# Performance work log

Hardware: AMD Instinct MI355X
Metric: run time of the kernel (lower is better)

The kernel has to match this reference:

```python
import jax, jax.numpy as jnp
import numpy as np

B = 4096
FEAT = 512
EMB = 64
HID = 1024
NUM_CLASSES = 64   # == option_num == noise_lib_Y.shape[0]
LIB_X = 256
LIB_Y = 256
OUT_J = 256


def setup_inputs() -> dict:
    key = jax.random.key(0)
    ks = jax.random.split(key, 16)
    s = lambda k, shape, fan: jax.random.normal(k, shape, jnp.float32) / np.sqrt(fan)
    d_in = FEAT + EMB
    return {
        "state": jax.random.normal(ks[0], (B, FEAT), jnp.float32),
        "option": jax.random.randint(ks[1], (B,), 0, NUM_CLASSES, jnp.int64),
        "embed_table": s(ks[2], (NUM_CLASSES, EMB), EMB),
        "Wx1": s(ks[3], (d_in, HID), d_in), "bx1": jnp.zeros((HID,), jnp.float32),
        "Wx2": s(ks[4], (HID, LIB_X), HID), "bx2": jnp.zeros((LIB_X,), jnp.float32),
        "Wy1": s(ks[5], (d_in, HID), d_in), "by1": jnp.zeros((HID,), jnp.float32),
        "Wy2": s(ks[6], (HID, LIB_Y), HID), "by2": jnp.zeros((LIB_Y,), jnp.float32),
        "noise_lib_X": s(ks[7], (LIB_X, OUT_J), LIB_X),
        "noise_lib_Y": s(ks[8], (NUM_CLASSES, LIB_Y, OUT_J), LIB_Y),
    }


def _mlp(x, W1, b1, W2, b2):
    # MLP_RELU, layer_num=2: Linear -> ReLU -> Linear
    h = jax.nn.relu(x @ W1 + b1)
    return h @ W2 + b2


def reference(state, option, embed_table, Wx1, bx1, Wx2, bx2,
              Wy1, by1, Wy2, by2, noise_lib_X, noise_lib_Y):
    option_embed = embed_table[option]                      # [B, EMB]
    all_state = jnp.concatenate([state, option_embed], axis=-1)
    cls_X = _mlp(all_state, Wx1, bx1, Wx2, bx2)             # [B, LIB_X]
    cls_Y = _mlp(all_state, Wy1, by1, Wy2, by2)             # [B, LIB_Y]
    # Original: einsum('bi,mij->bmj') then mask with one_hot(option).
    # Mathematically identical gather-then-matmul (honors the routing sparsity):
    noise_Y_sel = noise_lib_Y[option]                       # [B, LIB_Y, OUT_J]
    generate_noise_Y = jnp.einsum('bi,bij->bj', cls_Y, noise_Y_sel)
    generate_noise_X = cls_X @ noise_lib_X                  # [B, OUT_J]
    return (generate_noise_X, generate_noise_Y)
```

## Files before the change

kernel.cpp:

```cpp
#include <hip/hip_runtime.h>

typedef unsigned short u16;
typedef unsigned int u32;

using f32x4  = __attribute__((ext_vector_type(4))) float;
using bf16x8 = __attribute__((ext_vector_type(8))) __bf16;

#define DEV __device__ __forceinline__

DEV u16 f2bf(float f) {
  union { float f; u32 u; } x; x.f = f;
  return (u16)((x.u + 0x7fffu + ((x.u >> 16) & 1u)) >> 16);
}
DEV float bf2f(u16 h) {
  union { u32 u; float f; } x; x.u = ((u32)h) << 16;
  return x.f;
}

DEV void async_cp16(const u16* g, u16* l) {
  __builtin_amdgcn_global_load_lds((const __attribute__((address_space(1))) void*)g,
                                   (__attribute__((address_space(3))) void*)l,
                                   16, 0, 0);
}

static constexpr int BATCH = 4096;
static constexpr int FEAT  = 512;
static constexpr int EMB   = 64;
static constexpr int HID   = 1024;
static constexpr int NC    = 64;
static constexpr int DIN   = 576;
static constexpr int LIB   = 256;

DEV void detect_lite(const u32* __restrict__ sraw, const u32* __restrict__ oraw,
                     int* isf32, int* ostr) {
  __shared__ int cib, conz;
  const int t = threadIdx.x;
  if (t == 0) { cib = 0; conz = 0; }
  u32 w = sraw[t];
  u32 e = (w >> 7) & 0xFFu;
  unsigned long long m1 = __ballot(e >= 100 && e <= 142);
  unsigned long long m2 = __ballot((t & 1) && oraw[t] != 0);
  __syncthreads();
  if ((t & 63) == 0) {
    atomicAdd(&cib, __popcll(m1));
    atomicAdd(&conz, __popcll(m2));
  }
  __syncthreads();
  *isf32 = (cib < 128) ? 1 : 0;
  *ostr  = (conz == 0) ? 2 : 1;
}

DEV void load16_bf(u16* v, const void* __restrict__ in, size_t off, int isf32) {
  if (isf32) {
    const float4* s = (const float4*)((const float*)in + off);
    float4 a0 = s[0], a1 = s[1], a2 = s[2], a3 = s[3];
    v[0] = f2bf(a0.x); v[1] = f2bf(a0.y); v[2]  = f2bf(a0.z); v[3]  = f2bf(a0.w);
    v[4] = f2bf(a1.x); v[5] = f2bf(a1.y); v[6]  = f2bf(a1.z); v[7]  = f2bf(a1.w);
    v[8] = f2bf(a2.x); v[9] = f2bf(a2.y); v[10] = f2bf(a2.z); v[11] = f2bf(a2.w);
    v[12] = f2bf(a3.x); v[13] = f2bf(a3.y); v[14] = f2bf(a3.z); v[15] = f2bf(a3.w);
  } else {
    const uint4* s = (const uint4*)((const u16*)in + off);
    *(uint4*)&v[0] = s[0];
    *(uint4*)&v[8] = s[1];
  }
}

DEV void do_transpose64(u16* lds, const void* __restrict__ in,
                        u16* __restrict__ out, int R, int C,
                        int by, int bx, int isf32) {
  u16* tile = lds;
  const int t = threadIdx.x;
  {
    const int r = t >> 2, c0 = (t & 3) * 16;
    u16 v[16];
    load16_bf(v, in, (size_t)(by * 64 + r) * C + (bx * 64 + c0), isf32);
    *(uint4*)&tile[r * 72 + c0]     = *(uint4*)&v[0];
    *(uint4*)&tile[r * 72 + c0 + 8] = *(uint4*)&v[8];
  }
  __syncthreads();
  {
    const int c = t & 63, rs = (t >> 6) * 16;
    u16 w[16];
#pragma unroll
    for (int i = 0; i < 16; ++i) w[i] = tile[(rs + i) * 72 + c];
    size_t oo = (size_t)(bx * 64 + c) * R + (by * 64 + rs);
    *(uint4*)&out[oo]     = *(uint4*)&w[0];
    *(uint4*)&out[oo + 8] = *(uint4*)&w[8];
  }
}

DEV void tgemm_task(u16* lds, const void* __restrict__ nX,
                    const void* __restrict__ Wx2, u16* __restrict__ T,
                    int mt, int nt, int isf32) {
  u16* Als = lds;
  u16* Bls = lds + 64 * 72;
  const int t = threadIdx.x;
  const int m0 = mt * 64, q0 = nt * 64;
  const int lane = t & 63, wid = t >> 6;
  const int wm = wid >> 1, wn = wid & 1;
  const int lr = lane & 15, lq = lane >> 4;
  f32x4 acc[2][2] = {};
  for (int k0 = 0; k0 < LIB; k0 += 64) {
    __syncthreads();
    {
      const int r = t >> 2, c0 = (t & 3) * 16;
      u16 v[16];
      load16_bf(v, nX, (size_t)(k0 + r) * LIB + m0 + c0, isf32);
#pragma unroll
      for (int j = 0; j < 16; ++j) Als[(c0 + j) * 72 + r] = v[j];
      const int q = t >> 2, ic = (t & 3) * 16;
      u16 w16[16];
      load16_bf(w16, Wx2, (size_t)(q0 + q) * LIB + k0 + ic, isf32);
      u16* dst = &Bls[((ic >> 5) * 64 + q) * 32 + (ic & 31)];
      *(uint4*)dst       = *(uint4*)&w16[0];
      *(uint4*)(dst + 8) = *(uint4*)&w16[8];
    }
    __syncthreads();
#pragma unroll
    for (int sl = 0; sl < 2; ++sl) {
      bf16x8 av[2], bv[2];
#pragma unroll
      for (int i2 = 0; i2 < 2; ++i2)
        av[i2] = *(const bf16x8*)&Als[(wm * 32 + i2 * 16 + lr) * 72 + sl * 32 + lq * 8];
#pragma unroll
      for (int j2 = 0; j2 < 2; ++j2)
        bv[j2] = *(const bf16x8*)&Bls[(sl * 64 + wn * 32 + j2 * 16 + lr) * 32 + lq * 8];
#pragma unroll
      for (int i2 = 0; i2 < 2; ++i2)
#pragma unroll
        for (int j2 = 0; j2 < 2; ++j2)
          acc[i2][j2] = __builtin_amdgcn_mfma_f32_16x16x32_bf16(av[i2], bv[j2], acc[i2][j2], 0, 0, 0);
    }
  }
#pragma unroll
  for (int j2 = 0; j2 < 2; ++j2) {
    const int gc = q0 + wn * 32 + j2 * 16 + lr;
#pragma unroll
    for (int i2 = 0; i2 < 2; ++i2) {
      const int gr = m0 + wm * 32 + i2 * 16 + lq * 4;
#pragma unroll
      for (int r = 0; r < 4; ++r)
        T[(size_t)(gr + r) * HID + gc] = f2bf(acc[i2][j2][r]);
    }
  }
}

struct PrepArgs {
  const void *state, *emb, *Wx1, *Wy1, *Wy2, *Wx2, *nX, *bx2;
  const int* opt;
  u16 *all_state, *WT1x, *WT1y, *WT2y, *T;
  float* b2x;
};
static constexpr int PB_CONCAT = BATCH * 36 / 256;
static constexpr int PB_WT1 = (DIN / 64) * (HID / 64);
static constexpr int PB_WT2 = (HID / 64) * (LIB / 64);
static constexpr int PB_TG  = (LIB / 64) * (HID / 64);
static constexpr int PB_BIAS = 4;
static constexpr int PREP_BLOCKS = PB_CONCAT + 2 * PB_WT1 + PB_WT2 + PB_TG
                                 + PB_BIAS;

__global__ __launch_bounds__(256) void prep_k(PrepArgs a) {
  __shared__ __align__(16) u16 plds[64 * 72 + 128 * 32];
  __shared__ float red[4][64];
  int isf32, os;
  detect_lite((const u32*)a.state, (const u32*)a.opt, &isf32, &os);
  int bid = blockIdx.x;
  const int t = threadIdx.x;
  if (bid < PB_CONCAT) {
    int idx = bid * 256 + t;
    int b = idx / 36, ch = idx % 36;
    const void* base;
    size_t srcoff;
    if (ch < 32) { base = a.state; srcoff = (size_t)b * FEAT + ch * 16; }
    else {
      base = a.emb;
      srcoff = (size_t)a.opt[(size_t)b * os] * EMB + (ch - 32) * 16;
    }
    u16 o[16];
    load16_bf(o, base, srcoff, isf32);
    u16* dst = a.all_state + (size_t)b * DIN + ch * 16;
    *(uint4*)dst       = *(const uint4*)&o[0];
    *(uint4*)(dst + 8) = *(const uint4*)&o[8];
    return;
  }
  bid -= PB_CONCAT;
  if (bid < PB_WT1) { do_transpose64(plds, a.Wx1, a.WT1x, DIN, HID, bid >> 4, bid & 15, isf32); return; }
  bid -= PB_WT1;
  if (bid < PB_WT1) { do_transpose64(plds, a.Wy1, a.WT1y, DIN, HID, bid >> 4, bid & 15, isf32); return; }
  bid -= PB_WT1;
  if (bid < PB_WT2) { do_transpose64(plds, a.Wy2, a.WT2y, HID, LIB, bid >> 2, bid & 3, isf32); return; }
  bid -= PB_WT2;
  if (bid < PB_TG) { tgemm_task(plds, a.nX, a.Wx2, a.T, bid & 3, bid >> 2, isf32); return; }
  bid -= PB_TG;
  {
    const int j = bid * 64 + (t & 63), g = t >> 6;
    float acc = 0.f;
    for (int ii = 0; ii < 64; ++ii) {
      const int i = g * 64 + ii;
      float s = isf32 ? ((const float*)a.bx2)[i] : bf2f(((const u16*)a.bx2)[i]);
      float v = isf32 ? ((const float*)a.nX)[(size_t)i * LIB + j]
                      : bf2f(((const u16*)a.nX)[(size_t)i * LIB + j]);
      acc += s * v;
    }
    red[g][t & 63] = acc;
    __syncthreads();
    if (g == 0)
      a.b2x[j] = red[0][t & 63] + red[1][t & 63] + red[2][t & 63] + red[3][t & 63];
  }
}

template <int BM, int BN, bool RELU>
DEV void gemm_tile(u16* lds, const u16* __restrict__ A, const u16* __restrict__ Bt,
                   const void* bias, void* C, int N, int K, int m0, int n0,
                   int isf32, bool cf32, bool bf32) {
  constexpr int WM = BM / 2, WN = BN / 2, TM = WM / 16, TN = WN / 16;
  u16* As = lds;
  u16* Bs = lds + BM * 64;
  const int t = threadIdx.x;
  const int lane = t & 63, wid = t >> 6;
  const int wm = wid >> 1, wn = wid & 1;
  const int lr = lane & 15, lq = lane >> 4;
  f32x4 acc[TM][TN] = {};
  for (int k0 = 0; k0 < K; k0 += 64) {
    __syncthreads();
#pragma unroll
    for (int sl = 0; sl < 2; ++sl) {
#pragma unroll
      for (int u = 0; u < BM / 64; ++u) {
        int unit = u * 256 + t;
        int r = unit >> 2, c8 = (unit & 3) * 8;
        async_cp16(A + (size_t)(m0 + r) * K + (k0 + sl * 32 + c8),
                   &As[(sl * BM + r) * 32 + c8]);
      }
#pragma unroll
      for (int u = 0; u < BN / 64; ++u) {
        int unit = u * 256 + t;
        int r = unit >> 2, c8 = (unit & 3) * 8;
        async_cp16(Bt + (size_t)(n0 + r) * K + (k0 + sl * 32 + c8),
                   &Bs[(sl * BN + r) * 32 + c8]);
      }
    }
    __syncthreads();
#pragma unroll
    for (int sl = 0; sl < 2; ++sl) {
      bf16x8 av[TM], bv[TN];
#pragma unroll
      for (int i = 0; i < TM; ++i)
        av[i] = *(const bf16x8*)&As[(sl * BM + wm * WM + i * 16 + lr) * 32 + lq * 8];
#pragma unroll
      for (int j = 0; j < TN; ++j)
        bv[j] = *(const bf16x8*)&Bs[(sl * BN + wn * WN + j * 16 + lr) * 32 + lq * 8];
#pragma unroll
      for (int i = 0; i < TM; ++i)
#pragma unroll
        for (int j = 0; j < TN; ++j)
          acc[i][j] = __builtin_amdgcn_mfma_f32_16x16x32_bf16(av[i], bv[j], acc[i][j], 0, 0, 0);
    }
  }
#pragma unroll
  for (int j = 0; j < TN; ++j) {
    const int gc = n0 + wn * WN + j * 16 + lr;
    const float bval = bias
        ? (bf32 ? ((const float*)bias)[gc] : bf2f(((const u16*)bias)[gc]))
        : 0.f;
#pragma unroll
    for (int i = 0; i < TM; ++i) {
      const int gr = m0 + wm * WM + i * 16 + lq * 4;
#pragma unroll
      for (int r = 0; r < 4; ++r) {
        float v = acc[i][j][r] + bval;
        if (RELU) v = fmaxf(v, 0.f);
        const size_t idx = (size_t)(gr + r) * N + gc;
        if (cf32) ((float*)C)[idx] = v;
        else      ((u16*)C)[idx] = f2bf(v);
      }
    }
  }
}

struct GArg { const u16* A; const u16* Bt; const void* bias; void* C; int cflag; int bflag; };

template <int BM, int BN, bool RELU>
__global__ __launch_bounds__(256) void gemm_bt(GArg g0, GArg g1, int N, int K,
                                               const void* state, const void* opt) {
  __shared__ __align__(16) u16 lds[(BM + BN) * 64];
  int isf32, os;
  detect_lite((const u32*)state, (const u32*)opt, &isf32, &os);
  const GArg g = blockIdx.z ? g1 : g0;
  gemm_tile<BM, BN, RELU>(lds, g.A, g.Bt, g.bias, g.C, N, K,
                          blockIdx.y * BM, blockIdx.x * BN,
                          isf32, g.cflag && isf32, g.bflag || isf32);
}

struct TailArgs {
  const u16* cls_y;
  const void *nY, *state;
  const int* opt;
  void* out;
};

__global__ __launch_bounds__(256) void tail_k(TailArgs a) {
  __shared__ __align__(16) u16 lds[25216];
  __shared__ int wcnt[4], lbase;
  int isf32, os;
  detect_lite((const u32*)a.state, (const u32*)a.opt, &isf32, &os);
  const bool of32 = (isf32 != 0);
  const int t = threadIdx.x;
  const int lane = t & 63, w = t >> 6, lr = lane & 15, lq = lane >> 4;

  u16* Bts  = lds;
  u16* Asm  = lds + 16896;
  u16* list = lds + 21120;
  const int m = blockIdx.x >> 2, n0 = (blockIdx.x & 3) * 64;

#pragma unroll
  for (int pass = 0; pass < 4; ++pass) {
    const int k = pass * 64 + (t >> 2), nc = (t & 3) * 16;
    u16 v[16];
    load16_bf(v, a.nY, ((size_t)m * LIB + k) * LIB + n0 + nc, isf32);
#pragma unroll
    for (int j = 0; j < 16; ++j) Bts[(nc + j) * 264 + k] = v[j];
  }

  if (t == 0) lbase = 0;
  __syncthreads();
  for (int base = 0; base < BATCH; base += 256) {
    const int b = base + t;
    const int e = a.opt[(size_t)b * os];
    unsigned long long mk = __ballot(e == m);
    if (lane == 0) wcnt[w] = __popcll(mk);
    __syncthreads();
    int wpre = lbase;
    for (int i = 0; i < w; ++i) wpre += wcnt[i];
    const int mypre = __popcll(mk & ((1ull << lane) - 1ull));
    if (e == m) list[wpre + mypre] = (u16)b;
    __syncthreads();
    if (t == 0) lbase += wcnt[0] + wcnt[1] + wcnt[2] + wcnt[3];
  }
  __syncthreads();
  const int cnt = lbase;
  const size_t out_off = (size_t)BATCH * LIB;

  for (int ch = 0; ch < cnt; ch += 16) {
    __syncthreads();
    {
      const int r = t >> 4, cb = (t & 15) * 16;
      if (ch + r < cnt) {
        const u16* src = a.cls_y + (size_t)list[ch + r] * LIB + cb;
        *(uint4*)&Asm[r * 264 + cb]     = *(const uint4*)src;
        *(uint4*)&Asm[r * 264 + cb + 8] = *(const uint4*)(src + 8);
      } else {
        uint4 z{0, 0, 0, 0};
        *(uint4*)&Asm[r * 264 + cb]     = z;
        *(uint4*)&Asm[r * 264 + cb + 8] = z;
      }
    }
    __syncthreads();
    f32x4 acc = {};
#pragma unroll
    for (int kk = 0; kk < LIB; kk += 32) {
      bf16x8 av = *(const bf16x8*)&Asm[lr * 264 + kk + lq * 8];
      bf16x8 bv = *(const bf16x8*)&Bts[(w * 16 + lr) * 264 + kk + lq * 8];
      acc = __builtin_amdgcn_mfma_f32_16x16x32_bf16(av, bv, acc, 0, 0, 0);
    }
#pragma unroll
    for (int r = 0; r < 4; ++r) {
      const int rowc = lq * 4 + r;
      if (ch + rowc < cnt) {
        const size_t oi = out_off + (size_t)list[ch + rowc] * LIB
                        + (n0 + w * 16 + lr);
        if (of32) ((float*)a.out)[oi] = acc[r];
        else      ((u16*)a.out)[oi] = f2bf(acc[r]);
      }
    }
  }
}

extern "C" void kernel_launch(void* const* d_in, const int* in_sizes, int n_in,
                              void* d_out, int out_size, void* d_ws, size_t ws_size,
                              hipStream_t stream) {
  char* p = (char*)d_ws;
  auto alloc = [&](size_t bytes) { char* r = p; p += (bytes + 255) & ~(size_t)255; return r; };
  u16* all_state = (u16*)alloc((size_t)BATCH * DIN * 2);
  u16* h_x   = (u16*)alloc((size_t)BATCH * HID * 2);
  u16* h_y   = (u16*)alloc((size_t)BATCH * HID * 2);
  u16* cls_y = (u16*)alloc((size_t)BATCH * LIB * 2);
  u16* WT1x  = (u16*)alloc((size_t)HID * DIN * 2);
  u16* WT1y  = (u16*)alloc((size_t)HID * DIN * 2);
  u16* WT2y  = (u16*)alloc((size_t)LIB * HID * 2);
  u16* T     = (u16*)alloc((size_t)LIB * HID * 2);
  float* b2x = (float*)alloc((size_t)LIB * 4);

  const void* state = d_in[0];
  const void* opt   = d_in[1];

  PrepArgs pa;
  pa.state = state; pa.opt = (const int*)opt; pa.emb = d_in[2];
  pa.Wx1 = d_in[3]; pa.Wx2 = d_in[5]; pa.bx2 = d_in[6];
  pa.Wy1 = d_in[7]; pa.Wy2 = d_in[9]; pa.nX = d_in[11];
  pa.all_state = all_state; pa.WT1x = WT1x; pa.WT1y = WT1y; pa.WT2y = WT2y;
  pa.T = T; pa.b2x = b2x;
  prep_k<<<PREP_BLOCKS, 256, 0, stream>>>(pa);

  GArg g1x{all_state, WT1x, d_in[4], h_x, 0, 0};
  GArg g1y{all_state, WT1y, d_in[8], h_y, 0, 0};
  gemm_bt<128, 128, true><<<dim3(HID / 128, BATCH / 128, 2), 256, 0, stream>>>(
      g1x, g1y, HID, DIN, state, opt);

  GArg g2x{h_x, T, b2x, d_out, 1, 1};
  GArg g2y{h_y, WT2y, d_in[10], cls_y, 0, 0};
  gemm_bt<64, 64, false><<<dim3(LIB / 64, BATCH / 64, 2), 256, 0, stream>>>(
      g2x, g2y, LIB, HID, state, opt);

  TailArgs ta{cls_y, d_in[12], state, (const int*)opt, d_out};
  tail_k<<<256, 256, 0, stream>>>(ta);
}
```

Before: 155.3 us.

## Retune GEMM tiles and K-depth, use atomic list build in tail

The GEMM template gains a SLABS parameter so the K step per iteration can vary. The first GEMM now uses 128x64 tiles, giving twice as many blocks, and the second GEMM loads four 32-wide slabs per barrier pair instead of two. Separately, the tail kernel's per-option batch list is now built with per-wave atomicAdd on a shared counter instead of two block barriers per 256-row chunk. As a result the list order is no longer deterministic, and the larger slab depth raises LDS use per block.

```diff
diff --git a/kernel.cpp b/kernel.cpp
--- a/kernel.cpp
+++ b/kernel.cpp
@@ -209,22 +209,22 @@
   }
 }
 
-template <int BM, int BN, bool RELU>
+template <int BM, int BN, int SLABS, bool RELU>
 DEV void gemm_tile(u16* lds, const u16* __restrict__ A, const u16* __restrict__ Bt,
                    const void* bias, void* C, int N, int K, int m0, int n0,
                    int isf32, bool cf32, bool bf32) {
   constexpr int WM = BM / 2, WN = BN / 2, TM = WM / 16, TN = WN / 16;
   u16* As = lds;
-  u16* Bs = lds + BM * 64;
+  u16* Bs = lds + BM * 32 * SLABS;
   const int t = threadIdx.x;
   const int lane = t & 63, wid = t >> 6;
   const int wm = wid >> 1, wn = wid & 1;
   const int lr = lane & 15, lq = lane >> 4;
   f32x4 acc[TM][TN] = {};
-  for (int k0 = 0; k0 < K; k0 += 64) {
-    __syncthreads();
-#pragma unroll
-    for (int sl = 0; sl < 2; ++sl) {
+  for (int k0 = 0; k0 < K; k0 += 32 * SLABS) {
+    __syncthreads();
+#pragma unroll
+    for (int sl = 0; sl < SLABS; ++sl) {
 #pragma unroll
       for (int u = 0; u < BM / 64; ++u) {
         int unit = u * 256 + t;
@@ -242,7 +242,7 @@
     }
     __syncthreads();
 #pragma unroll
-    for (int sl = 0; sl < 2; ++sl) {
+    for (int sl = 0; sl < SLABS; ++sl) {
       bf16x8 av[TM], bv[TN];
 #pragma unroll
       for (int i = 0; i < TM; ++i)
@@ -280,16 +280,16 @@
 
 struct GArg { const u16* A; const u16* Bt; const void* bias; void* C; int cflag; int bflag; };
 
-template <int BM, int BN, bool RELU>
+template <int BM, int BN, int SLABS, bool RELU>
 __global__ __launch_bounds__(256) void gemm_bt(GArg g0, GArg g1, int N, int K,
                                                const void* state, const void* opt) {
-  __shared__ __align__(16) u16 lds[(BM + BN) * 64];
+  __shared__ __align__(16) u16 lds[(BM + BN) * 32 * SLABS];
   int isf32, os;
   detect_lite((const u32*)state, (const u32*)opt, &isf32, &os);
   const GArg g = blockIdx.z ? g1 : g0;
-  gemm_tile<BM, BN, RELU>(lds, g.A, g.Bt, g.bias, g.C, N, K,
-                          blockIdx.y * BM, blockIdx.x * BN,
-                          isf32, g.cflag && isf32, g.bflag || isf32);
+  gemm_tile<BM, BN, SLABS, RELU>(lds, g.A, g.Bt, g.bias, g.C, N, K,
+                                 blockIdx.y * BM, blockIdx.x * BN,
+                                 isf32, g.cflag && isf32, g.bflag || isf32);
 }
 
 struct TailArgs {
@@ -301,7 +301,7 @@
 
 __global__ __launch_bounds__(256) void tail_k(TailArgs a) {
   __shared__ __align__(16) u16 lds[25216];
-  __shared__ int wcnt[4], lbase;
+  __shared__ int lcnt;
   int isf32, os;
   detect_lite((const u32*)a.state, (const u32*)a.opt, &isf32, &os);
   const bool of32 = (isf32 != 0);
@@ -312,6 +312,7 @@
   u16* Asm  = lds + 16896;
   u16* list = lds + 21120;
   const int m = blockIdx.x >> 2, n0 = (blockIdx.x & 3) * 64;
+  if (t == 0) lcnt = 0;
 
 #pragma unroll
   for (int pass = 0; pass < 4; ++pass) {
@@ -322,23 +323,20 @@
     for (int j = 0; j < 16; ++j) Bts[(nc + j) * 264 + k] = v[j];
   }
 
-  if (t == 0) lbase = 0;
   __syncthreads();
   for (int base = 0; base < BATCH; base += 256) {
     const int b = base + t;
     const int e = a.opt[(size_t)b * os];
     unsigned long long mk = __ballot(e == m);
-    if (lane == 0) wcnt[w] = __popcll(mk);
-    __syncthreads();
-    int wpre = lbase;
-    for (int i = 0; i < w; ++i) wpre += wcnt[i];
+    const int nw = __popcll(mk);
+    int wbase = 0;
+    if (lane == 0 && nw) wbase = atomicAdd(&lcnt, nw);
+    wbase = __shfl(wbase, 0);
     const int mypre = __popcll(mk & ((1ull << lane) - 1ull));
-    if (e == m) list[wpre + mypre] = (u16)b;
-    __syncthreads();
-    if (t == 0) lbase += wcnt[0] + wcnt[1] + wcnt[2] + wcnt[3];
+    if (e == m) list[wbase + mypre] = (u16)b;
   }
   __syncthreads();
-  const int cnt = lbase;
+  const int cnt = lcnt;
   const size_t out_off = (size_t)BATCH * LIB;
 
   for (int ch = 0; ch < cnt; ch += 16) {
@@ -404,12 +402,12 @@
 
   GArg g1x{all_state, WT1x, d_in[4], h_x, 0, 0};
   GArg g1y{all_state, WT1y, d_in[8], h_y, 0, 0};
-  gemm_bt<128, 128, true><<<dim3(HID / 128, BATCH / 128, 2), 256, 0, stream>>>(
+  gemm_bt<128, 64, 2, true><<<dim3(HID / 64, BATCH / 128, 2), 256, 0, stream>>>(
       g1x, g1y, HID, DIN, state, opt);
 
   GArg g2x{h_x, T, b2x, d_out, 1, 1};
   GArg g2y{h_y, WT2y, d_in[10], cls_y, 0, 0};
-  gemm_bt<64, 64, false><<<dim3(LIB / 64, BATCH / 64, 2), 256, 0, stream>>>(
+  gemm_bt<64, 64, 4, false><<<dim3(LIB / 64, BATCH / 64, 2), 256, 0, stream>>>(
       g2x, g2y, LIB, HID, state, opt);
 
   TailArgs ta{cls_y, d_in[12], state, (const int*)opt, d_out};
```

New measurement: 152.4 us. Within noise of the previous version (-1.9%).
